# Optimization experiments

Measured on AMD Instinct MI355X. Metric: run time of the kernel, lower is better.

## Reference

```python
import jax, jax.numpy as jnp
import numpy as np

B, S, V, E, H, L = 32, 512, 32000, 256, 512, 48


def setup_inputs() -> dict:
    key = jax.random.key(0)
    ks = jax.random.split(key, 12)
    tokens = jax.random.randint(ks[0], (B, S), 0, V)
    length = jax.random.randint(ks[1], (B,), S // 2, S + 1)
    labels = jax.random.randint(ks[2], (B, S), 0, L)
    embed_table = jax.random.normal(ks[3], (V, E), jnp.float32) * 0.1
    embed_table = embed_table.at[0].set(0.0)  # padding_idx = 0
    # torch LSTM gate order: i, f, g, o ; b = b_ih + b_hh folded together
    w_ih_f = jax.random.normal(ks[4], (4 * H, E), jnp.float32) * 0.05
    w_hh_f = jax.random.normal(ks[5], (4 * H, H), jnp.float32) * 0.05
    b_f = jnp.zeros((4 * H,), jnp.float32)
    w_ih_b = jax.random.normal(ks[6], (4 * H, E), jnp.float32) * 0.05
    w_hh_b = jax.random.normal(ks[7], (4 * H, H), jnp.float32) * 0.05
    b_b = jnp.zeros((4 * H,), jnp.float32)
    w_em = jax.random.normal(ks[8], (L, 2 * H), jnp.float32) * 0.02
    b_em = jnp.zeros((L,), jnp.float32)
    transition = jax.random.uniform(ks[9], (L, L), jnp.float32)  # torch.rand init
    return {"tokens": tokens, "length": length, "labels": labels,
            "embed_table": embed_table,
            "w_ih_f": w_ih_f, "w_hh_f": w_hh_f, "b_f": b_f,
            "w_ih_b": w_ih_b, "w_hh_b": w_hh_b, "b_b": b_b,
            "w_em": w_em, "b_em": b_em, "transition": transition}


def _lstm_dir(x, w_ih, w_hh, b, reverse):
    # x: [B,S,E] -> hidden states [B,S,H]
    xw = jnp.einsum('bse,ge->bsg', x, w_ih) + b  # precompute input projection [B,S,4H]
    if reverse:
        xw = xw[:, ::-1]
    Bn = x.shape[0]
    Hn = w_hh.shape[1]
    h0 = jnp.zeros((Bn, Hn), x.dtype)
    c0 = jnp.zeros((Bn, Hn), x.dtype)

    def step(carry, xt):
        h, c = carry
        gates = xt + h @ w_hh.T  # [B,4H]
        i, f, g, o = jnp.split(gates, 4, axis=-1)
        i = jax.nn.sigmoid(i)
        f = jax.nn.sigmoid(f)
        g = jnp.tanh(g)
        o = jax.nn.sigmoid(o)
        c = f * c + i * g
        h = o * jnp.tanh(c)
        return (h, c), h

    _, hs = jax.lax.scan(step, (h0, c0), jnp.swapaxes(xw, 0, 1))
    hs = jnp.swapaxes(hs, 0, 1)  # [B,S,H]
    if reverse:
        hs = hs[:, ::-1]
    return hs


def reference(tokens, length, labels, embed_table,
              w_ih_f, w_hh_f, b_f, w_ih_b, w_hh_b, b_b,
              w_em, b_em, transition):
    x = embed_table[tokens]                      # [B,S,E]
    hf = _lstm_dir(x, w_ih_f, w_hh_f, b_f, reverse=False)
    hb = _lstm_dir(x, w_ih_b, w_hh_b, b_b, reverse=True)
    h = jnp.concatenate([hf, hb], axis=-1)       # [B,S,2H]
    logits = jnp.einsum('bsh,lh->bsl', h, w_em) + b_em
    e = jnp.exp(logits)                          # emission = exp(linear), as in source
    T = jnp.exp(transition)                      # transition = exp(param), as in source
    Bn, Sn = tokens.shape
    pos = jnp.arange(Sn)[None, :]
    mask = pos < length[:, None]                 # [B,S] valid positions

    # gold path score: sum emissions over valid steps + transitions between them
    em_real = jnp.take_along_axis(e, labels[..., None], axis=-1)[..., 0]  # [B,S]
    real = jnp.sum(em_real * mask, axis=-1)
    trans_real = T[labels[:, :-1], labels[:, 1:]]                          # [B,S-1]
    real = real + jnp.sum(trans_real * mask[:, 1:], axis=-1)

    # forward algorithm, exactly as written in source:
    # alpha_new[k] = logsumexp_l( alpha[k] + T[k,l] + e_t[l] )
    alpha0 = e[:, 0, :]                          # [B,L]

    def step(alpha, inp):
        et, mt = inp                             # [B,L], [B]
        scores = alpha[:, :, None] + T[None, :, :] + et[:, None, :]  # [B,L,L]
        new = jax.nn.logsumexp(scores, axis=-1)
        alpha = jnp.where(mt[:, None], new, alpha)
        return alpha, None

    alpha, _ = jax.lax.scan(step, alpha0,
                            (jnp.swapaxes(e[:, 1:], 0, 1),
                             jnp.swapaxes(mask[:, 1:], 0, 1)))
    sum_score = jax.nn.logsumexp(alpha, axis=-1)  # [B]
    return sum_score - real                       # negative log probability per example
```

## Files before the change

### kernel.cpp

```cpp
#include <hip/hip_runtime.h>
#include <math.h>
#include <stdint.h>

#define Bn 32
#define Sn 512
#define En 256
#define Hn 512
#define Ln 48
#define G4 2048
#define NWG 32
#define SENT16 0x7FFFu

typedef unsigned short u16;
typedef __attribute__((ext_vector_type(8))) __bf16 bf16x8;
typedef __attribute__((ext_vector_type(4))) float f32x4;

__device__ inline float bf2f(u16 u) {
    return __uint_as_float(((unsigned)u) << 16);
}
__device__ inline u16 f2bf(float f) {
    unsigned u = __float_as_uint(f);
    unsigned r = (u + 0x7fffu + ((u >> 16) & 1u)) >> 16;
    return (u16)r;
}
__device__ inline float sigmoidf_(float x) { return 1.f / (1.f + expf(-x)); }
__device__ inline float tanh_fast(float x) { return 2.f / (1.f + expf(-2.f * x)) - 1.f; }

__device__ inline int chunkBad(f32x4 v) {
    unsigned x0 = __float_as_uint(v.x), x1 = __float_as_uint(v.y);
    unsigned x2 = __float_as_uint(v.z), x3 = __float_as_uint(v.w);
    int bad = 0;
    bad |= ((x0 & 0xFFFFu) == SENT16) | ((x0 >> 16) == SENT16);
    bad |= ((x1 & 0xFFFFu) == SENT16) | ((x1 >> 16) == SENT16);
    bad |= ((x2 & 0xFFFFu) == SENT16) | ((x2 >> 16) == SENT16);
    bad |= ((x3 & 0xFFFFu) == SENT16) | ((x3 >> 16) == SENT16);
    return bad;
}

__global__ __launch_bounds__(256) void prep_kernel(
    const int* __restrict__ tokens, const float* __restrict__ embed,
    const float* __restrict__ wihf, const float* __restrict__ wihb,
    const float* __restrict__ whhf, const float* __restrict__ whhb,
    const float* __restrict__ wem, const float* __restrict__ trans,
    u16* __restrict__ xbf, u16* __restrict__ wihf_b, u16* __restrict__ wihb_b,
    u16* __restrict__ whhf_b, u16* __restrict__ whhb_b, u16* __restrict__ wem_b,
    float* __restrict__ expT, float* __restrict__ alphaAcc,
    float* __restrict__ realAcc, unsigned* __restrict__ hf32,
    unsigned* __restrict__ hb32)
{
    size_t idx = (size_t)blockIdx.x * blockDim.x + threadIdx.x;
    size_t stride = (size_t)gridDim.x * blockDim.x;
    for (size_t i = idx; i < (size_t)Bn * Sn * En; i += stride) {
        size_t n = i >> 8; int ee = (int)(i & 255);
        int tok = tokens[n];
        xbf[i] = f2bf(embed[(size_t)tok * En + ee]);
    }
    for (size_t i = idx; i < (size_t)G4 * En; i += stride) {
        wihf_b[i] = f2bf(wihf[i]); wihb_b[i] = f2bf(wihb[i]);
    }
    for (size_t i = idx; i < (size_t)G4 * Hn; i += stride) {
        whhf_b[i] = f2bf(whhf[i]); whhb_b[i] = f2bf(whhb[i]);
    }
    for (size_t i = idx; i < (size_t)Ln * 2 * Hn; i += stride) wem_b[i] = f2bf(wem[i]);
    for (size_t i = idx; i < (size_t)Ln * Ln; i += stride) expT[i] = expf(trans[i]);
    for (size_t i = idx; i < (size_t)Bn * Ln; i += stride) alphaAcc[i] = 0.f;
    for (size_t i = idx; i < (size_t)Bn; i += stride) realAcc[i] = 0.f;
    const unsigned sp = (SENT16 << 16) | SENT16;
    for (size_t i = idx; i < (size_t)Bn * Sn * Hn / 2; i += stride) {
        hf32[i] = sp; hb32[i] = sp;
    }
}

__global__ __launch_bounds__(256) void gemm_xw(
    const u16* __restrict__ xbf, const u16* __restrict__ wihf_b,
    const u16* __restrict__ wihb_b, const float* __restrict__ bias_f,
    const float* __restrict__ bias_b, u16* __restrict__ xw_f, u16* __restrict__ xw_b)
{
    int mb = blockIdx.x, nb = blockIdx.y, dir = blockIdx.z;
    const u16* wih = dir ? wihb_b : wihf_b;
    const float* bias = dir ? bias_b : bias_f;
    u16* xw = dir ? xw_b : xw_f;

    __shared__ u16 At[64 * 136];
    __shared__ u16 Bt[64 * 136];

    int tid = threadIdx.x;
    int w = tid >> 6, lane = tid & 63;
    int lm = lane & 15, lkq = (lane >> 4) * 8;
    int Moff = (w & 1) * 32, Noff = (w >> 1) * 32;

    f32x4 zero = {0.f, 0.f, 0.f, 0.f};
    f32x4 acc[2][2] = {{zero, zero}, {zero, zero}};

    for (int kc = 0; kc < 2; kc++) {
        for (int c = tid; c < 1024; c += 256) {
            int r = c >> 4, cc = (c & 15) * 8;
            *(bf16x8*)&At[r * 136 + cc] =
                *(const bf16x8*)&xbf[((size_t)(mb * 64 + r)) * En + kc * 128 + cc];
            *(bf16x8*)&Bt[r * 136 + cc] =
                *(const bf16x8*)&wih[((size_t)(nb * 64 + r)) * En + kc * 128 + cc];
        }
        __syncthreads();
        #pragma unroll
        for (int ks = 0; ks < 4; ks++) {
            int k = ks * 32 + lkq;
            bf16x8 a0 = *(const bf16x8*)&At[(Moff + lm) * 136 + k];
            bf16x8 a1 = *(const bf16x8*)&At[(Moff + 16 + lm) * 136 + k];
            bf16x8 b0 = *(const bf16x8*)&Bt[(Noff + lm) * 136 + k];
            bf16x8 b1 = *(const bf16x8*)&Bt[(Noff + 16 + lm) * 136 + k];
            acc[0][0] = __builtin_amdgcn_mfma_f32_16x16x32_bf16(a0, b0, acc[0][0], 0, 0, 0);
            acc[0][1] = __builtin_amdgcn_mfma_f32_16x16x32_bf16(a0, b1, acc[0][1], 0, 0, 0);
            acc[1][0] = __builtin_amdgcn_mfma_f32_16x16x32_bf16(a1, b0, acc[1][0], 0, 0, 0);
            acc[1][1] = __builtin_amdgcn_mfma_f32_16x16x32_bf16(a1, b1, acc[1][1], 0, 0, 0);
        }
        __syncthreads();
    }
    #pragma unroll
    for (int mi = 0; mi < 2; mi++)
        #pragma unroll
        for (int ni = 0; ni < 2; ni++)
            #pragma unroll
            for (int reg = 0; reg < 4; reg++) {
                int row = Moff + mi * 16 + (lane >> 4) * 4 + reg;
                int col = Noff + ni * 16 + lm;
                int n = mb * 64 + row;
                int g = nb * 64 + col;
                int t = n & 511, b = n >> 9;
                float v = acc[mi][ni][reg] + bias[g];
                xw[((size_t)t * Bn + b) * G4 + g] = f2bf(v);
            }
}

__global__ __launch_bounds__(512) void lstm_rec(
    const u16* __restrict__ whhf_b, const u16* __restrict__ whhb_b,
    const u16* __restrict__ xw_f, const u16* __restrict__ xw_b,
    u16* __restrict__ hf, u16* __restrict__ hb)
{
    int wg = blockIdx.x;
    int dir = wg >> 5;
    int w = wg & 31;
    const u16* __restrict__ whh = dir ? whhb_b : whhf_b;
    const u16* __restrict__ xw  = dir ? xw_b  : xw_f;
    u16* __restrict__ hbuf = dir ? hb : hf;

    __shared__ u16 Hs[32 * 512];
    __shared__ float Cp[4 * 32 * 17];
    __shared__ u16 hout[32 * 16];

    int tid = threadIdx.x;
    int wv = tid >> 6, lane = tid & 63;
    int lm = lane & 15, kq = lane >> 4;
    int mt = wv & 1, nt = wv >> 1;
    int b = tid >> 4, hc = tid & 15;

    bf16x8 Bf[16];
    {
        const u16* wrow = &whh[((size_t)nt * Hn + (size_t)w * 16 + lm) * Hn];
        #pragma unroll
        for (int ks = 0; ks < 16; ks++)
            Bf[ks] = *(const bf16x8*)&wrow[ks * 32 + kq * 8];
    }

    float c_state = 0.f;
    const f32x4 zero = {0.f, 0.f, 0.f, 0.f};

    for (int it = 0; it < Sn; it++) {
        int t = dir ? (Sn - 1 - it) : it;
        f32x4 acc = zero;

        const u16* xp = &xw[((size_t)t * Bn + b) * G4 + (size_t)w * 16 + hc];
        float xg0 = bf2f(xp[0 * Hn]);
        float xg1 = bf2f(xp[1 * Hn]);
        float xg2 = bf2f(xp[2 * Hn]);
        float xg3 = bf2f(xp[3 * Hn]);

        if (it > 0) {
            int tprev = dir ? (t + 1) : (t - 1);
            const u16* base = &hbuf[((size_t)b * Sn + tprev) * Hn];
            const u16* p0 = base + (hc + 0) * 8;
            const u16* p1 = base + (hc + 16) * 8;
            const u16* p2 = base + (hc + 32) * 8;
            const u16* p3 = base + (hc + 48) * 8;
            f32x4 h0, h1, h2, h3;
            int tries = 0;
            while (true) {
                asm volatile(
                    "global_load_dwordx4 %0, %4, off sc0 sc1\n\t"
                    "global_load_dwordx4 %1, %5, off sc0 sc1\n\t"
                    "global_load_dwordx4 %2, %6, off sc0 sc1\n\t"
                    "global_load_dwordx4 %3, %7, off sc0 sc1\n\t"
                    "s_waitcnt vmcnt(0)"
                    : "=v"(h0), "=v"(h1), "=v"(h2), "=v"(h3)
                    : "v"(p0), "v"(p1), "v"(p2), "v"(p3)
                    : "memory");
                if (!(chunkBad(h0) | chunkBad(h1) | chunkBad(h2) | chunkBad(h3))) break;
                if (++tries > 65536) break;
            }
            *(f32x4*)&Hs[(b * 64 + ((hc + 0) ^ (b & 7))) * 8] = h0;
            *(f32x4*)&Hs[(b * 64 + ((hc + 16) ^ (b & 7))) * 8] = h1;
            *(f32x4*)&Hs[(b * 64 + ((hc + 32) ^ (b & 7))) * 8] = h2;
            *(f32x4*)&Hs[(b * 64 + ((hc + 48) ^ (b & 7))) * 8] = h3;
            __syncthreads();
            #pragma unroll
            for (int ks = 0; ks < 16; ks++) {
                bf16x8 a = *(const bf16x8*)
                    &Hs[((mt * 16 + lm) * 64 + ((ks * 4 + kq) ^ (lm & 7))) * 8];
                acc = __builtin_amdgcn_mfma_f32_16x16x32_bf16(a, Bf[ks], acc, 0, 0, 0);
            }
        }

        #pragma unroll
        for (int reg = 0; reg < 4; reg++)
            Cp[(nt * 32 + mt * 16 + kq * 4 + reg) * 17 + lm] = acc[reg];
        __syncthreads();

        float g0 = Cp[(0 * 32 + b) * 17 + hc] + xg0;
        float g1 = Cp[(1 * 32 + b) * 17 + hc] + xg1;
        float g2 = Cp[(2 * 32 + b) * 17 + hc] + xg2;
        float g3 = Cp[(3 * 32 + b) * 17 + hc] + xg3;
        float i_ = sigmoidf_(g0);
        float f_ = sigmoidf_(g1);
        float gg = tanh_fast(g2);
        float o_ = sigmoidf_(g3);
        c_state = f_ * c_state + i_ * gg;
        float hv = o_ * tanh_fast(c_state);
        hout[tid] = f2bf(hv);
        __syncthreads();

        if (tid < 64) {
            int bq = lane >> 1, half = lane & 1;
            f32x4 hv8 = *(const f32x4*)&hout[lane * 8];
            u16* sp = &hbuf[((size_t)bq * Sn + t) * Hn + (size_t)w * 16 + half * 8];
            asm volatile("global_store_dwordx4 %0, %1, off sc0 sc1"
                         :: "v"(sp), "v"(hv8) : "memory");
        }
    }
}

__global__ __launch_bounds__(256) void emis(
    const u16* __restrict__ hf, const u16* __restrict__ hb,
    const u16* __restrict__ wem_b, const float* __restrict__ bem,
    float* __restrict__ e)
{
    int mb = blockIdx.x;
    int tid = threadIdx.x, wv = tid >> 6, lane = tid & 63;
    int lm = lane & 15, lkq = (lane >> 4) * 8;
    int row = mb * 64 + wv * 16;

    f32x4 zero = {0.f, 0.f, 0.f, 0.f};
    f32x4 acc[3] = {zero, zero, zero};
    for (int ks = 0; ks < 32; ks++) {
        int k = ks * 32 + lkq;
        const u16* hsrc = (ks < 16) ? &hf[(size_t)(row + lm) * Hn + k]
                                    : &hb[(size_t)(row + lm) * Hn + (k - 512)];
        bf16x8 a = *(const bf16x8*)hsrc;
        #pragma unroll
        for (int nt = 0; nt < 3; nt++) {
            bf16x8 bfr = *(const bf16x8*)&wem_b[(size_t)(nt * 16 + lm) * 1024 + k];
            acc[nt] = __builtin_amdgcn_mfma_f32_16x16x32_bf16(a, bfr, acc[nt], 0, 0, 0);
        }
    }
    #pragma unroll
    for (int nt = 0; nt < 3; nt++)
        #pragma unroll
        for (int reg = 0; reg < 4; reg++) {
            int r = row + (lane >> 4) * 4 + reg;
            int col = nt * 16 + lm;
            float lg = acc[nt][reg] + bem[col];
            e[(size_t)r * Ln + col] = expf(lg);
        }
}

__global__ __launch_bounds__(64) void crf_step(
    const float* __restrict__ e, const float* __restrict__ expT,
    const int* __restrict__ labels, const int* __restrict__ lengths,
    float* __restrict__ alphaAcc, float* __restrict__ realAcc)
{
    int bt = blockIdx.x;
    int b = bt >> 9, t = bt & 511;
    __shared__ float er[Ln];
    int tid = threadIdx.x;
    if (tid < Ln) er[tid] = e[(size_t)bt * Ln + tid];
    __syncthreads();
    bool inlen = t < lengths[b];
    if (t >= 1 && inlen && tid < Ln) {
        int i = tid;
        float m = -1e30f;
        for (int j = 0; j < Ln; j++) m = fmaxf(m, expT[i * Ln + j] + er[j]);
        float s = 0.f;
        for (int j = 0; j < Ln; j++) s += expf(expT[i * Ln + j] + er[j] - m);
        atomicAdd(&alphaAcc[b * Ln + i], m + logf(s));
    }
    if (tid == 0 && inlen) {
        int lab = labels[b * Sn + t];
        float r = er[lab];
        if (t >= 1) r += expT[labels[b * Sn + t - 1] * Ln + lab];
        atomicAdd(&realAcc[b], r);
    }
}

__global__ __launch_bounds__(64) void finalize(
    const float* __restrict__ e, const float* __restrict__ alphaAcc,
    const float* __restrict__ realAcc, float* __restrict__ out)
{
    int b = threadIdx.x;
    if (b >= Bn) return;
    float m = -1e30f;
    for (int i = 0; i < Ln; i++) {
        float a = e[((size_t)b * Sn) * Ln + i] + alphaAcc[b * Ln + i];
        m = fmaxf(m, a);
    }
    float s = 0.f;
    for (int i = 0; i < Ln; i++) {
        float a = e[((size_t)b * Sn) * Ln + i] + alphaAcc[b * Ln + i];
        s += expf(a - m);
    }
    out[b] = m + logf(s) - realAcc[b];
}

extern "C" void kernel_launch(void* const* d_in, const int* in_sizes, int n_in,
                              void* d_out, int out_size, void* d_ws, size_t ws_size,
                              hipStream_t stream)
{
    const int*   tokens = (const int*)d_in[0];
    const int*   length = (const int*)d_in[1];
    const int*   labels = (const int*)d_in[2];
    const float* embed  = (const float*)d_in[3];
    const float* wihf   = (const float*)d_in[4];
    const float* whhf   = (const float*)d_in[5];
    const float* bf     = (const float*)d_in[6];
    const float* wihb   = (const float*)d_in[7];
    const float* whhb   = (const float*)d_in[8];
    const float* bbv    = (const float*)d_in[9];
    const float* wem    = (const float*)d_in[10];
    const float* bem    = (const float*)d_in[11];
    const float* trans  = (const float*)d_in[12];
    float* out = (float*)d_out;

    char* p = (char*)d_ws;
    auto take = [&](size_t bytes) -> char* {
        char* q = p;
        p += (bytes + 255) & ~(size_t)255;
        return q;
    };
    u16* xw_f   = (u16*)take((size_t)Sn * Bn * G4 * 2);
    u16* xw_b   = (u16*)take((size_t)Sn * Bn * G4 * 2);
    u16* hf     = (u16*)take((size_t)Bn * Sn * Hn * 2);
    u16* hb     = (u16*)take((size_t)Bn * Sn * Hn * 2);
    u16* xbf    = (u16*)take((size_t)Bn * Sn * En * 2);
    u16* wihf_b = (u16*)take((size_t)G4 * En * 2);
    u16* wihb_b = (u16*)take((size_t)G4 * En * 2);
    u16* whhf_b = (u16*)take((size_t)G4 * Hn * 2);
    u16* whhb_b = (u16*)take((size_t)G4 * Hn * 2);
    u16* wem_b  = (u16*)take((size_t)Ln * 2 * Hn * 2);
    float* e        = (float*)take((size_t)Bn * Sn * Ln * 4);
    float* expT     = (float*)take((size_t)Ln * Ln * 4);
    float* alphaAcc = (float*)take((size_t)Bn * Ln * 4);
    float* realAcc  = (float*)take((size_t)Bn * 4);
    if ((size_t)(p - (char*)d_ws) > ws_size) return;

    prep_kernel<<<4096, 256, 0, stream>>>(tokens, embed, wihf, wihb, whhf, whhb, wem, trans,
                                          xbf, wihf_b, wihb_b, whhf_b, whhb_b, wem_b,
                                          expT, alphaAcc, realAcc,
                                          (unsigned*)hf, (unsigned*)hb);

    dim3 g1(256, 32, 2);
    gemm_xw<<<g1, 256, 0, stream>>>(xbf, wihf_b, wihb_b, bf, bbv, xw_f, xw_b);

    void* ra[] = { (void*)&whhf_b, (void*)&whhb_b, (void*)&xw_f, (void*)&xw_b,
                   (void*)&hf, (void*)&hb };
    hipLaunchCooperativeKernel((const void*)lstm_rec, dim3(2 * NWG), dim3(512), ra, 0, stream);

    emis<<<256, 256, 0, stream>>>(hf, hb, wem_b, bem, e);
    crf_step<<<Bn * Sn, 64, 0, stream>>>(e, expT, labels, length, alphaAcc, realAcc);
    finalize<<<1, 64, 0, stream>>>(e, alphaAcc, realAcc, out);
}
```

Measured before the change: 1.920 ms.

## Pipeline sentinel polling loads, split MFMA chains, store h directly per thread

The cross-workgroup spin-wait on the previous hidden state now double-buffers its polling loads, issuing the next batch before checking the current one, and uses a cheaper SWAR sentinel test. The MFMA reduction is split into two independent accumulator chains to shorten the dependency latency. The LDS staging of h plus the extra __syncthreads before the global store is replaced by one 2-byte store per thread, which removes a barrier from each timestep. The cost is more outstanding polling traffic and many small uncoalesced stores in place of a few 16-byte stores.

```diff
diff --git a/kernel.cpp b/kernel.cpp
--- a/kernel.cpp
+++ b/kernel.cpp
@@ -26,15 +26,15 @@
 __device__ inline float sigmoidf_(float x) { return 1.f / (1.f + expf(-x)); }
 __device__ inline float tanh_fast(float x) { return 2.f / (1.f + expf(-2.f * x)) - 1.f; }
 
-__device__ inline int chunkBad(f32x4 v) {
-    unsigned x0 = __float_as_uint(v.x), x1 = __float_as_uint(v.y);
-    unsigned x2 = __float_as_uint(v.z), x3 = __float_as_uint(v.w);
-    int bad = 0;
-    bad |= ((x0 & 0xFFFFu) == SENT16) | ((x0 >> 16) == SENT16);
-    bad |= ((x1 & 0xFFFFu) == SENT16) | ((x1 >> 16) == SENT16);
-    bad |= ((x2 & 0xFFFFu) == SENT16) | ((x2 >> 16) == SENT16);
-    bad |= ((x3 & 0xFFFFu) == SENT16) | ((x3 >> 16) == SENT16);
-    return bad;
+__device__ inline unsigned badMask(f32x4 v) {
+    unsigned acc = 0;
+    #pragma unroll
+    for (int i = 0; i < 4; i++) {
+        unsigned d = __float_as_uint(v[i]);
+        unsigned x = d ^ 0x7FFF7FFFu;
+        acc |= (x - 0x00010001u) & ~x & 0x80008000u;
+    }
+    return acc;
 }
 
 __global__ __launch_bounds__(256) void prep_kernel(
@@ -145,7 +145,6 @@
 
     __shared__ u16 Hs[32 * 512];
     __shared__ float Cp[4 * 32 * 17];
-    __shared__ u16 hout[32 * 16];
 
     int tid = threadIdx.x;
     int wv = tid >> 6, lane = tid & 63;
@@ -163,6 +162,8 @@
 
     float c_state = 0.f;
     const f32x4 zero = {0.f, 0.f, 0.f, 0.f};
+    const float sentf = __uint_as_float(0x7FFF7FFFu);
+    const f32x4 sentv = {sentf, sentf, sentf, sentf};
 
     for (int it = 0; it < Sn; it++) {
         int t = dir ? (Sn - 1 - it) : it;
@@ -181,32 +182,47 @@
             const u16* p1 = base + (hc + 16) * 8;
             const u16* p2 = base + (hc + 32) * 8;
             const u16* p3 = base + (hc + 48) * 8;
-            f32x4 h0, h1, h2, h3;
-            int tries = 0;
+
+            f32x4 A0 = sentv, A1 = sentv, A2 = sentv, A3 = sentv;
+            f32x4 B0 = sentv, B1 = sentv, B2 = sentv, B3 = sentv;
+            #define LD4(d, p) asm volatile("global_load_dwordx4 %0, %1, off sc0 sc1" \
+                                           : "+v"(d) : "v"(p))
+            LD4(A0, p0); LD4(A1, p1); LD4(A2, p2); LD4(A3, p3);
+            int useB = 0, tries = 0;
             while (true) {
-                asm volatile(
-                    "global_load_dwordx4 %0, %4, off sc0 sc1\n\t"
-                    "global_load_dwordx4 %1, %5, off sc0 sc1\n\t"
-                    "global_load_dwordx4 %2, %6, off sc0 sc1\n\t"
-                    "global_load_dwordx4 %3, %7, off sc0 sc1\n\t"
-                    "s_waitcnt vmcnt(0)"
-                    : "=v"(h0), "=v"(h1), "=v"(h2), "=v"(h3)
-                    : "v"(p0), "v"(p1), "v"(p2), "v"(p3)
-                    : "memory");
-                if (!(chunkBad(h0) | chunkBad(h1) | chunkBad(h2) | chunkBad(h3))) break;
-                if (++tries > 65536) break;
+                LD4(B0, p0); LD4(B1, p1); LD4(B2, p2); LD4(B3, p3);
+                asm volatile("s_waitcnt vmcnt(4)"
+                             : "+v"(A0), "+v"(A1), "+v"(A2), "+v"(A3));
+                if (!(badMask(A0) | badMask(A1) | badMask(A2) | badMask(A3))) { useB = 0; break; }
+                LD4(A0, p0); LD4(A1, p1); LD4(A2, p2); LD4(A3, p3);
+                asm volatile("s_waitcnt vmcnt(4)"
+                             : "+v"(B0), "+v"(B1), "+v"(B2), "+v"(B3));
+                if (!(badMask(B0) | badMask(B1) | badMask(B2) | badMask(B3))) { useB = 1; break; }
+                if ((tries += 2) > (1 << 18)) break;
             }
-            *(f32x4*)&Hs[(b * 64 + ((hc + 0) ^ (b & 7))) * 8] = h0;
-            *(f32x4*)&Hs[(b * 64 + ((hc + 16) ^ (b & 7))) * 8] = h1;
-            *(f32x4*)&Hs[(b * 64 + ((hc + 32) ^ (b & 7))) * 8] = h2;
-            *(f32x4*)&Hs[(b * 64 + ((hc + 48) ^ (b & 7))) * 8] = h3;
+            asm volatile("s_waitcnt vmcnt(0)"
+                         : "+v"(A0), "+v"(A1), "+v"(A2), "+v"(A3),
+                           "+v"(B0), "+v"(B1), "+v"(B2), "+v"(B3) : : "memory");
+            if (useB) { A0 = B0; A1 = B1; A2 = B2; A3 = B3; }
+            #undef LD4
+
+            *(f32x4*)&Hs[(b * 64 + ((hc + 0) ^ (b & 7))) * 8] = A0;
+            *(f32x4*)&Hs[(b * 64 + ((hc + 16) ^ (b & 7))) * 8] = A1;
+            *(f32x4*)&Hs[(b * 64 + ((hc + 32) ^ (b & 7))) * 8] = A2;
+            *(f32x4*)&Hs[(b * 64 + ((hc + 48) ^ (b & 7))) * 8] = A3;
             __syncthreads();
+
+            f32x4 aa = zero, ab = zero;
             #pragma unroll
-            for (int ks = 0; ks < 16; ks++) {
-                bf16x8 a = *(const bf16x8*)
-                    &Hs[((mt * 16 + lm) * 64 + ((ks * 4 + kq) ^ (lm & 7))) * 8];
-                acc = __builtin_amdgcn_mfma_f32_16x16x32_bf16(a, Bf[ks], acc, 0, 0, 0);
+            for (int ks2 = 0; ks2 < 8; ks2++) {
+                bf16x8 a0 = *(const bf16x8*)
+                    &Hs[((mt * 16 + lm) * 64 + (((2 * ks2) * 4 + kq) ^ (lm & 7))) * 8];
+                aa = __builtin_amdgcn_mfma_f32_16x16x32_bf16(a0, Bf[2 * ks2], aa, 0, 0, 0);
+                bf16x8 a1 = *(const bf16x8*)
+                    &Hs[((mt * 16 + lm) * 64 + (((2 * ks2 + 1) * 4 + kq) ^ (lm & 7))) * 8];
+                ab = __builtin_amdgcn_mfma_f32_16x16x32_bf16(a1, Bf[2 * ks2 + 1], ab, 0, 0, 0);
             }
+            acc = aa + ab;
         }
 
         #pragma unroll
@@ -224,16 +240,11 @@
         float o_ = sigmoidf_(g3);
         c_state = f_ * c_state + i_ * gg;
         float hv = o_ * tanh_fast(c_state);
-        hout[tid] = f2bf(hv);
-        __syncthreads();
-
-        if (tid < 64) {
-            int bq = lane >> 1, half = lane & 1;
-            f32x4 hv8 = *(const f32x4*)&hout[lane * 8];
-            u16* sp = &hbuf[((size_t)bq * Sn + t) * Hn + (size_t)w * 16 + half * 8];
-            asm volatile("global_store_dwordx4 %0, %1, off sc0 sc1"
-                         :: "v"(sp), "v"(hv8) : "memory");
-        }
+
+        unsigned hval = (unsigned)f2bf(hv);
+        u16* spH = &hbuf[((size_t)b * Sn + t) * Hn + (size_t)w * 16 + hc];
+        asm volatile("global_store_short %0, %1, off sc0 sc1"
+                     :: "v"(spH), "v"(hval) : "memory");
     }
 }
 
```

After: 2.500 ms. 30.2% more time.
